# Performance work log

Hardware: AMD Instinct MI355X
Metric: run time of the kernel (lower is better)

The kernel has to match this reference:

```python
import jax, jax.numpy as jnp
import numpy as np

N_NODES = 50000
N_EDGES = 800000
D_IN = 128
D_SH = 16
D_OUT = 128
N_PATHS = 64


def setup_inputs() -> dict:
    key = jax.random.key(0)
    k1, k2, k3, k4, k5, k6, k7, k8 = jax.random.split(key, 8)
    x = jax.random.normal(k1, (N_NODES, D_IN), dtype=jnp.float32)
    sh = jax.random.normal(k2, (N_EDGES, D_SH), dtype=jnp.float32)
    coeff = jax.random.normal(k3, (N_PATHS,), dtype=jnp.float32)
    src = jax.random.randint(k4, (N_EDGES,), 0, N_NODES, dtype=jnp.int64)
    dst = jax.random.randint(k5, (N_EDGES,), 0, N_NODES, dtype=jnp.int64)
    ki = jax.random.randint(k6, (N_PATHS,), 0, D_IN, dtype=jnp.int32)
    kj = jax.random.randint(k7, (N_PATHS,), 0, D_SH, dtype=jnp.int32)
    ko = jax.random.randint(k8, (N_PATHS,), 0, D_OUT, dtype=jnp.int32)
    return {"x": x, "sh": sh, "coeff": coeff, "src": src, "dst": dst,
            "ki": ki, "kj": kj, "ko": ko}


def reference(x, sh, coeff, src, dst, ki, kj, ko):
    # 1) gather: index_select node features by edge source -> [E, D_in]
    xg = x[src]
    # 2) segmented tensor product: sum over sparse paths p of
    #    coeff[p] * xg[:, ki[p]] * sh[:, kj[p]] accumulated into output slot ko[p]
    vals = coeff[None, :] * xg[:, ki] * sh[:, kj]          # [E, P]
    msg = jnp.zeros((sh.shape[0], D_OUT), dtype=x.dtype).at[:, ko].add(vals)  # [E, D_out]
    # 3) scatter_add messages into per-node output -> [N, D_out]
    out = jnp.zeros((x.shape[0], D_OUT), dtype=x.dtype).at[dst].add(msg)
    return out
```

## Files before the change

### kernel.cpp

```cpp
#include <hip/hip_runtime.h>
#include <hip/hip_fp16.h>

#define N_NODES 50000
#define N_EDGES 800000
#define D_IN    128
#define D_SH    16
#define D_OUT   128
#define N_PATHS 64
#define CAP     64
#define BLK     256
#define EBLK    (N_EDGES / BLK)
#define NODE_B  (N_NODES / 4)

#define OFF_BUK 200000
#define OFF_XCH (OFF_BUK + 25600000)
#define WS_NEED ((size_t)OFF_XCH + 6400000)

__global__ __launch_bounds__(BLK) void build_kernel(
        const float* __restrict__ x, const int* __restrict__ ki,
        const int* __restrict__ src, const int* __restrict__ dst,
        int* __restrict__ cnt, int2* __restrict__ bucket,
        __half* __restrict__ xc_h) {
    if (blockIdx.x < EBLK) {
        int e = blockIdx.x * BLK + threadIdx.x;
        int d = dst[e];
        int pos = atomicAdd(&cnt[d], 1);
        if (pos < CAP)
            bucket[(size_t)d * CAP + pos] = make_int2(e, src[e]);
    } else {
        const int b    = blockIdx.x - EBLK;
        const int lane = threadIdx.x & 63;
        const int w    = threadIdx.x >> 6;
        const int n    = b * 4 + w;
        xc_h[(size_t)n * N_PATHS + lane] =
            __float2half_rn(x[(size_t)n * D_IN + ki[lane]]);
    }
}

__global__ __launch_bounds__(BLK) void node_kernel(
        const float* __restrict__ sh, const __half* __restrict__ xc_h,
        const int* __restrict__ cnt, const int2* __restrict__ bucket,
        const float* __restrict__ coeff, const int* __restrict__ kj,
        const int* __restrict__ ko, float* __restrict__ out) {
    __shared__ float srow[BLK / 64][D_OUT];
    const int lane = threadIdx.x & 63;
    const int w    = threadIdx.x >> 6;
    const int node = blockIdx.x * 4 + w;

    const int   kj_p = kj[lane];
    const int   ko_p = ko[lane];
    const float c_p  = coeff[lane];

    const int cnt_n = min(cnt[node], CAP);
    int2 pp = bucket[(size_t)node * CAP + lane];
    int e_l = pp.x, s_l = pp.y;

    float acc = 0.0f;
    int j = 0;
    for (; j + 4 <= cnt_n; j += 4) {
        int e0 = __shfl(e_l, j    ), s0 = __shfl(s_l, j    );
        int e1 = __shfl(e_l, j + 1), s1 = __shfl(s_l, j + 1);
        int e2 = __shfl(e_l, j + 2), s2 = __shfl(s_l, j + 2);
        int e3 = __shfl(e_l, j + 3), s3 = __shfl(s_l, j + 3);
        float x0 = __half2float(xc_h[(size_t)s0 * N_PATHS + lane]);
        float v0 = sh[(size_t)e0 * D_SH + kj_p];
        float x1 = __half2float(xc_h[(size_t)s1 * N_PATHS + lane]);
        float v1 = sh[(size_t)e1 * D_SH + kj_p];
        float x2 = __half2float(xc_h[(size_t)s2 * N_PATHS + lane]);
        float v2 = sh[(size_t)e2 * D_SH + kj_p];
        float x3 = __half2float(xc_h[(size_t)s3 * N_PATHS + lane]);
        float v3 = sh[(size_t)e3 * D_SH + kj_p];
        acc += x0 * v0; acc += x1 * v1; acc += x2 * v2; acc += x3 * v3;
    }
    for (; j < cnt_n; ++j) {
        int e0 = __shfl(e_l, j), s0 = __shfl(s_l, j);
        acc += __half2float(xc_h[(size_t)s0 * N_PATHS + lane])
             * sh[(size_t)e0 * D_SH + kj_p];
    }
    acc *= c_p;

    srow[w][lane]      = 0.0f;
    srow[w][lane + 64] = 0.0f;
    __syncthreads();
    atomicAdd(&srow[w][ko_p], acc);
    __syncthreads();
    float* orow = out + (size_t)node * D_OUT;
    orow[lane]      = srow[w][lane];
    orow[lane + 64] = srow[w][lane + 64];
}

extern "C" void kernel_launch(void* const* d_in, const int* in_sizes, int n_in,
                              void* d_out, int out_size, void* d_ws, size_t ws_size,
                              hipStream_t stream) {
    const float* x     = (const float*)d_in[0];
    const float* sh    = (const float*)d_in[1];
    const float* coeff = (const float*)d_in[2];
    const int*   src   = (const int*)d_in[3];
    const int*   dst   = (const int*)d_in[4];
    const int*   ki    = (const int*)d_in[5];
    const int*   kj    = (const int*)d_in[6];
    const int*   ko    = (const int*)d_in[7];
    float* out = (float*)d_out;

    char* p = (char*)d_ws;
    int*    cnt    = (int*)p;
    int2*   bucket = (int2*)(p + OFF_BUK);
    __half* xc_h   = (__half*)(p + OFF_XCH);
    (void)ws_size;

    hipMemsetAsync(cnt, 0, (size_t)N_NODES * sizeof(int), stream);
    build_kernel<<<EBLK + NODE_B, BLK, 0, stream>>>(
        x, ki, src, dst, cnt, bucket, xc_h);
    node_kernel<<<NODE_B, BLK, 0, stream>>>(
        sh, xc_h, cnt, bucket, coeff, kj, ko, out);
}
```

Measured before the change: 225.3 us.

## Chunk bucket layout, vectorize edge scatter, unroll gather by 8, drop block syncs

The bucket storage becomes a chunked layout (16 slots per node per chunk, chunks strided by node count), so only occupied slots are touched and sparse nodes read compact lines. The scatter phase handles four edges per thread with int4 loads of src/dst, and the x-compaction phase does four nodes per wave. The node kernel loads only valid bucket slots, uses readlane instead of shfl, unrolls the gather by 8 with a masked tail, and removes the __syncthreads around the per-wave shared-memory reduction, relying on wave-level execution order. This trades fewer instructions and less bucket traffic for a reliance on implicit wave synchronisation of LDS atomics.

```diff
diff --git a/kernel.cpp b/kernel.cpp
--- a/kernel.cpp
+++ b/kernel.cpp
@@ -8,32 +8,56 @@
 #define D_OUT   128
 #define N_PATHS 64
 #define CAP     64
+#define CHUNK   16
 #define BLK     256
-#define EBLK    (N_EDGES / BLK)
+
+#define SCAT_T  (N_EDGES / 4)
+#define SCAT_B  ((SCAT_T + BLK - 1) / BLK)
+#define XC_B    (N_NODES / 16)
 #define NODE_B  (N_NODES / 4)
 
 #define OFF_BUK 200000
 #define OFF_XCH (OFF_BUK + 25600000)
 #define WS_NEED ((size_t)OFF_XCH + 6400000)
 
+__device__ __forceinline__ size_t bslot(int d, int pos) {
+    return ((size_t)(pos >> 4) * N_NODES + d) * CHUNK + (pos & 15);
+}
+
 __global__ __launch_bounds__(BLK) void build_kernel(
         const float* __restrict__ x, const int* __restrict__ ki,
         const int* __restrict__ src, const int* __restrict__ dst,
         int* __restrict__ cnt, int2* __restrict__ bucket,
         __half* __restrict__ xc_h) {
-    if (blockIdx.x < EBLK) {
-        int e = blockIdx.x * BLK + threadIdx.x;
-        int d = dst[e];
-        int pos = atomicAdd(&cnt[d], 1);
-        if (pos < CAP)
-            bucket[(size_t)d * CAP + pos] = make_int2(e, src[e]);
+    if (blockIdx.x < SCAT_B) {
+        int idx = blockIdx.x * BLK + threadIdx.x;
+        if (idx < SCAT_T) {
+            int4 s4 = ((const int4*)src)[idx];
+            int4 d4 = ((const int4*)dst)[idx];
+            int e0 = idx * 4;
+            int p0 = atomicAdd(&cnt[d4.x], 1);
+            int p1 = atomicAdd(&cnt[d4.y], 1);
+            int p2 = atomicAdd(&cnt[d4.z], 1);
+            int p3 = atomicAdd(&cnt[d4.w], 1);
+            if (p0 < CAP) bucket[bslot(d4.x, p0)] = make_int2(e0,     s4.x);
+            if (p1 < CAP) bucket[bslot(d4.y, p1)] = make_int2(e0 + 1, s4.y);
+            if (p2 < CAP) bucket[bslot(d4.z, p2)] = make_int2(e0 + 2, s4.z);
+            if (p3 < CAP) bucket[bslot(d4.w, p3)] = make_int2(e0 + 3, s4.w);
+        }
     } else {
-        const int b    = blockIdx.x - EBLK;
+        const int b2   = blockIdx.x - SCAT_B;
         const int lane = threadIdx.x & 63;
         const int w    = threadIdx.x >> 6;
-        const int n    = b * 4 + w;
-        xc_h[(size_t)n * N_PATHS + lane] =
-            __float2half_rn(x[(size_t)n * D_IN + ki[lane]]);
+        const int nb   = b2 * 16 + w * 4;
+        const int kil  = ki[lane];
+        float x0 = x[(size_t)(nb + 0) * D_IN + kil];
+        float x1 = x[(size_t)(nb + 1) * D_IN + kil];
+        float x2 = x[(size_t)(nb + 2) * D_IN + kil];
+        float x3 = x[(size_t)(nb + 3) * D_IN + kil];
+        xc_h[(size_t)(nb + 0) * N_PATHS + lane] = __float2half_rn(x0);
+        xc_h[(size_t)(nb + 1) * N_PATHS + lane] = __float2half_rn(x1);
+        xc_h[(size_t)(nb + 2) * N_PATHS + lane] = __float2half_rn(x2);
+        xc_h[(size_t)(nb + 3) * N_PATHS + lane] = __float2half_rn(x3);
     }
 }
 
@@ -51,42 +75,53 @@
     const int   ko_p = ko[lane];
     const float c_p  = coeff[lane];
 
-    const int cnt_n = min(cnt[node], CAP);
-    int2 pp = bucket[(size_t)node * CAP + lane];
-    int e_l = pp.x, s_l = pp.y;
+    const int cnt_n = __builtin_amdgcn_readfirstlane(min(cnt[node], CAP));
+
+    int e_l = 0, s_l = 0;
+    if (lane < cnt_n) {
+        int2 pp = bucket[bslot(node, lane)];
+        e_l = pp.x; s_l = pp.y;
+    }
 
     float acc = 0.0f;
     int j = 0;
-    for (; j + 4 <= cnt_n; j += 4) {
-        int e0 = __shfl(e_l, j    ), s0 = __shfl(s_l, j    );
-        int e1 = __shfl(e_l, j + 1), s1 = __shfl(s_l, j + 1);
-        int e2 = __shfl(e_l, j + 2), s2 = __shfl(s_l, j + 2);
-        int e3 = __shfl(e_l, j + 3), s3 = __shfl(s_l, j + 3);
-        float x0 = __half2float(xc_h[(size_t)s0 * N_PATHS + lane]);
-        float v0 = sh[(size_t)e0 * D_SH + kj_p];
-        float x1 = __half2float(xc_h[(size_t)s1 * N_PATHS + lane]);
-        float v1 = sh[(size_t)e1 * D_SH + kj_p];
-        float x2 = __half2float(xc_h[(size_t)s2 * N_PATHS + lane]);
-        float v2 = sh[(size_t)e2 * D_SH + kj_p];
-        float x3 = __half2float(xc_h[(size_t)s3 * N_PATHS + lane]);
-        float v3 = sh[(size_t)e3 * D_SH + kj_p];
-        acc += x0 * v0; acc += x1 * v1; acc += x2 * v2; acc += x3 * v3;
+    for (; j + 8 <= cnt_n; j += 8) {
+        float xv[8], sv[8];
+        #pragma unroll
+        for (int u = 0; u < 8; ++u) {
+            int e = __builtin_amdgcn_readlane(e_l, j + u);
+            int s = __builtin_amdgcn_readlane(s_l, j + u);
+            xv[u] = __half2float(xc_h[(size_t)s * N_PATHS + lane]);
+            sv[u] = sh[(size_t)e * D_SH + kj_p];
+        }
+        #pragma unroll
+        for (int u = 0; u < 8; ++u) acc += xv[u] * sv[u];
     }
-    for (; j < cnt_n; ++j) {
-        int e0 = __shfl(e_l, j), s0 = __shfl(s_l, j);
-        acc += __half2float(xc_h[(size_t)s0 * N_PATHS + lane])
-             * sh[(size_t)e0 * D_SH + kj_p];
+    if (j < cnt_n) {
+        float xv[8], sv[8];
+        #pragma unroll
+        for (int u = 0; u < 8; ++u) {
+            int jj = j + u;
+            int jc = jj < cnt_n ? jj : 0;
+            int e = __builtin_amdgcn_readlane(e_l, jc);
+            int s = __builtin_amdgcn_readlane(s_l, jc);
+            xv[u] = __half2float(xc_h[(size_t)s * N_PATHS + lane]);
+            sv[u] = sh[(size_t)e * D_SH + kj_p];
+        }
+        #pragma unroll
+        for (int u = 0; u < 8; ++u)
+            if (j + u < cnt_n) acc += xv[u] * sv[u];
     }
     acc *= c_p;
 
     srow[w][lane]      = 0.0f;
     srow[w][lane + 64] = 0.0f;
-    __syncthreads();
     atomicAdd(&srow[w][ko_p], acc);
-    __syncthreads();
+    float r0 = srow[w][lane];
+    float r1 = srow[w][lane + 64];
     float* orow = out + (size_t)node * D_OUT;
-    orow[lane]      = srow[w][lane];
-    orow[lane + 64] = srow[w][lane + 64];
+    orow[lane]      = r0;
+    orow[lane + 64] = r1;
 }
 
 extern "C" void kernel_launch(void* const* d_in, const int* in_sizes, int n_in,
@@ -109,7 +144,7 @@
     (void)ws_size;
 
     hipMemsetAsync(cnt, 0, (size_t)N_NODES * sizeof(int), stream);
-    build_kernel<<<EBLK + NODE_B, BLK, 0, stream>>>(
+    build_kernel<<<SCAT_B + XC_B, BLK, 0, stream>>>(
         x, ki, src, dst, cnt, bucket, xc_h);
     node_kernel<<<NODE_B, BLK, 0, stream>>>(
         sh, xc_h, cnt, bucket, coeff, kj, ko, out);
```

After: 220.6 us. 2.1% less time.
